# Kernel optimization log

Hardware: AMD Instinct MI355X
Metric: run time of the kernel (lower is better)

Reference implementation:

```python
import jax, jax.numpy as jnp
import numpy as np

B = 1048576          # batch size
N_IN = 10            # input features
NQ = 3               # n_qubits
NM = 2               # n_fuzzy_mem
NC = NM ** NQ        # 8 fuzzy combinations
EPS_GN = 1e-5
EPS_BN = 1e-5
CLAMP = 0.99999

# bit pattern per combination: loc[j] is the j-th digit (MSB first) of i in binary
SEL = jnp.array([[(i >> 2) & 1, (i >> 1) & 1, i & 1] for i in range(NC)], dtype=jnp.int32)  # [8,3]


def setup_inputs() -> dict:
    key = jax.random.key(0)
    ks = jax.random.split(key, 12)
    x = jax.random.normal(ks[0], (B, N_IN), dtype=jnp.float32)
    # linear 10->3 (xavier-ish scale), bias init 0.01 per weights_init
    W1 = jax.random.normal(ks[1], (NQ, N_IN), dtype=jnp.float32) * (1.0 / np.sqrt(N_IN))
    b1 = jnp.full((NQ,), 0.01, dtype=jnp.float32)
    # GroupNorm(1,3) affine
    gamma = jnp.ones((NQ,), dtype=jnp.float32)
    beta = jnp.zeros((NQ,), dtype=jnp.float32)
    # fuzzy membership params m, theta ~ N(0,1), shape [n_qubits, n_fuzzy_mem]
    m = jax.random.normal(ks[2], (NQ, NM), dtype=jnp.float32)
    theta = jax.random.normal(ks[3], (NQ, NM), dtype=jnp.float32)
    # BatchNorm1d(8) affine
    gamma2 = jnp.ones((NC,), dtype=jnp.float32)
    beta2 = jnp.zeros((NC,), dtype=jnp.float32)
    # softmax_linear 8->10
    W2 = jax.random.normal(ks[4], (N_IN, NC), dtype=jnp.float32) * (1.0 / np.sqrt(NC))
    b2 = jnp.full((N_IN,), 0.01, dtype=jnp.float32)
    return {"x": x, "W1": W1, "b1": b1, "gamma": gamma, "beta": beta,
            "m": m, "theta": theta, "gamma2": gamma2, "beta2": beta2,
            "W2": W2, "b2": b2}


def reference(x, W1, b1, gamma, beta, m, theta, gamma2, beta2, W2, b2):
    # linear 10 -> 3
    h = x @ W1.T + b1                                   # [B,3]
    # GroupNorm(1,3): per-sample normalization over channels (biased var)
    mu = h.mean(axis=1, keepdims=True)
    var = ((h - mu) ** 2).mean(axis=1, keepdims=True)
    h = (h - mu) * jax.lax.rsqrt(var + EPS_GN) * gamma + beta
    # gaussian fuzzy memberships: [B, n_mem=2, n_qubits=3]
    mT = m.T[None]                                      # [1,2,3]
    tT = theta.T[None]                                  # [1,2,3]
    fuzzy = jnp.exp(-((h[:, None, :] - mT) ** 2) / (2.0 * tT ** 2))  # [B,2,3]
    # select membership per combination: q_in[b,i,j] = fuzzy[b, SEL[i,j], j]
    q_in = fuzzy[:, SEL, jnp.arange(NQ)]                # [B,8,3]
    # RY angle = 2*arcsin(clamp(sqrt(q+1e-16))); per-qubit P(|1>) = sin^2(angle/2)
    sq = jnp.clip(jnp.sqrt(q_in + 1e-16), None, CLAMP)
    p = sq * sq                                         # [B,8,3]
    # 5-qubit circuit RY,RY,RY + CCX(0,1,3) + CCX(2,3,4); probs[1] = P(q0=1,q1=0,q2=0)
    out = p[..., 0] * (1.0 - p[..., 1]) * (1.0 - p[..., 2])  # [B,8]
    # BatchNorm1d(8), training mode (batch stats, biased var)
    mu2 = out.mean(axis=0)
    var2 = ((out - mu2) ** 2).mean(axis=0)
    out = (out - mu2) * jax.lax.rsqrt(var2 + EPS_BN) * gamma2 + beta2
    # softmax_linear 8 -> 10
    logits = out @ W2.T + b2                            # [B,10]
    # q_defuzz: 3-qubit RY circuit on first 3 logits; probs[0..2]
    s = jnp.sin(logits[:, :NQ] * 0.5)
    pq = s * s                                          # P(q_i=1), [B,3]
    cq = 1.0 - pq
    res = jnp.stack([cq[:, 0] * cq[:, 1] * cq[:, 2],
                     pq[:, 0] * cq[:, 1] * cq[:, 2],
                     cq[:, 0] * pq[:, 1] * cq[:, 2]], axis=1)  # [B,3]
    return res
```

## Files before the change

kernel.cpp:

```cpp
#include <hip/hip_runtime.h>

#define NROWS   1048576
#define NPAIRS  (NROWS / 2)
#define PMAX    0.9999800001f

#define P1_BLOCKS 1024
#define P1_THREADS 256
#define P2_BLOCKS (NPAIRS / 256)

__device__ __forceinline__ void fill_w(float* w, int t,
        const float* __restrict__ W1, const float* __restrict__ b1,
        const float* __restrict__ gamma, const float* __restrict__ beta,
        const float* __restrict__ mm, const float* __restrict__ theta) {
    if (t < 30) w[t] = W1[t];
    else if (t < 33) w[t] = b1[t - 30];
    else if (t < 39) { int k = t - 33; w[t] = (mm[k] - beta[k >> 1]) / gamma[k >> 1]; }
    else if (t < 45) { int k = t - 39; float g = gamma[k >> 1], th = theta[k];
                       w[t] = g * g / (2.0f * th * th); }
}

__device__ __forceinline__ void row_out(const float* xr, const float* w, float* o) {
    float h0 = w[30], h1 = w[31], h2 = w[32];
#pragma unroll
    for (int i = 0; i < 10; ++i) {
        h0 = fmaf(xr[i], w[i],      h0);
        h1 = fmaf(xr[i], w[10 + i], h1);
        h2 = fmaf(xr[i], w[20 + i], h2);
    }
    float mu = (h0 + h1 + h2) * (1.0f / 3.0f);
    float d0 = h0 - mu, d1 = h1 - mu, d2 = h2 - mu;
    float rs = rsqrtf((d0 * d0 + d1 * d1 + d2 * d2) * (1.0f / 3.0f) + 1e-5f);
    float u[3] = {d0 * rs, d1 * rs, d2 * rs};
    float P[3][2];
#pragma unroll
    for (int q = 0; q < 3; ++q)
#pragma unroll
        for (int s = 0; s < 2; ++s) {
            float d = u[q] - w[33 + q * 2 + s];
            float e = __expf(-(d * d) * w[39 + q * 2 + s]);
            P[q][s] = fminf(e + 1e-16f, PMAX);
        }
    float A0 = P[0][0], A1 = P[0][1];
    float B0 = 1.0f - P[1][0], B1 = 1.0f - P[1][1];
    float C0 = 1.0f - P[2][0], C1 = 1.0f - P[2][1];
    o[0] = A0 * B0 * C0; o[1] = A0 * B0 * C1; o[2] = A0 * B1 * C0; o[3] = A0 * B1 * C1;
    o[4] = A1 * B0 * C0; o[5] = A1 * B0 * C1; o[6] = A1 * B1 * C0; o[7] = A1 * B1 * C1;
}

__device__ __forceinline__ void load_pair(const float* __restrict__ x, int p, float* xr) {
    const float4* xv = reinterpret_cast<const float4*>(x) + (size_t)p * 5;
    float4 v0 = xv[0], v1 = xv[1], v2 = xv[2], v3 = xv[3], v4 = xv[4];
    xr[0] = v0.x; xr[1] = v0.y; xr[2] = v0.z; xr[3] = v0.w;
    xr[4] = v1.x; xr[5] = v1.y; xr[6] = v1.z; xr[7] = v1.w;
    xr[8] = v2.x; xr[9] = v2.y; xr[10] = v2.z; xr[11] = v2.w;
    xr[12] = v3.x; xr[13] = v3.y; xr[14] = v3.z; xr[15] = v3.w;
    xr[16] = v4.x; xr[17] = v4.y; xr[18] = v4.z; xr[19] = v4.w;
}

__global__ __launch_bounds__(256) void k_pass1(const float* __restrict__ x,
        const float* __restrict__ W1, const float* __restrict__ b1,
        const float* __restrict__ gamma, const float* __restrict__ beta,
        const float* __restrict__ mm, const float* __restrict__ theta,
        float* __restrict__ ws) {
    __shared__ float w[45];
    __shared__ float red[256][17];
    __shared__ float red2[16][17];
    int t = threadIdx.x;
    fill_w(w, t, W1, b1, gamma, beta, mm, theta);
    __syncthreads();

    float rw[45];
#pragma unroll
    for (int i = 0; i < 45; ++i) rw[i] = w[i];

    float s[8], ss[8];
#pragma unroll
    for (int c = 0; c < 8; ++c) { s[c] = 0.0f; ss[c] = 0.0f; }

    int tid = blockIdx.x * P1_THREADS + t;
    const int nthreads = P1_BLOCKS * P1_THREADS;
#pragma unroll
    for (int it = 0; it < 2; ++it) {
        int p = tid + it * nthreads;
        float xr[20];
        load_pair(x, p, xr);
        float o[8];
        row_out(xr, rw, o);
#pragma unroll
        for (int c = 0; c < 8; ++c) { s[c] += o[c]; ss[c] = fmaf(o[c], o[c], ss[c]); }
        row_out(xr + 10, rw, o);
#pragma unroll
        for (int c = 0; c < 8; ++c) { s[c] += o[c]; ss[c] = fmaf(o[c], o[c], ss[c]); }
    }

#pragma unroll
    for (int c = 0; c < 8; ++c) { red[t][c] = s[c]; red[t][8 + c] = ss[c]; }
    __syncthreads();
    {
        int c16 = t & 15, g = t >> 4;
        float partial = 0.0f;
#pragma unroll
        for (int j = 0; j < 16; ++j) partial += red[g * 16 + j][c16];
        red2[g][c16] = partial;
    }
    __syncthreads();
    if (t < 16) {
        float f = 0.0f;
#pragma unroll
        for (int g = 0; g < 16; ++g) f += red2[g][t];
        atomicAdd(&ws[(blockIdx.x & 15) * 16 + t], f);
    }
}

__global__ __launch_bounds__(256) void k_pass2(const float* __restrict__ x,
        const float* __restrict__ W1, const float* __restrict__ b1,
        const float* __restrict__ gamma, const float* __restrict__ beta,
        const float* __restrict__ mm, const float* __restrict__ theta,
        const float* __restrict__ g2, const float* __restrict__ be2,
        const float* __restrict__ W2, const float* __restrict__ b2,
        const float* __restrict__ ws, float* __restrict__ res) {
    __shared__ float w[45];
    __shared__ float weff[27];
    __shared__ float a8[8], sh8[8];
    int t = threadIdx.x;
    fill_w(w, t, W1, b1, gamma, beta, mm, theta);
    if (t >= 64 && t < 72) {
        int c = t - 64;
        float sv = 0.0f, qv = 0.0f;
#pragma unroll
        for (int r = 0; r < 16; ++r) { sv += ws[r * 16 + c]; qv += ws[r * 16 + 8 + c]; }
        const float invB = 1.0f / (float)NROWS;
        float mu = sv * invB;
        float var = qv * invB - mu * mu;
        float ac = g2[c] * rsqrtf(var + 1e-5f);
        a8[c] = ac;
        sh8[c] = be2[c] - mu * ac;
    }
    __syncthreads();
    if (t < 3) {
        float c0 = b2[t];
#pragma unroll
        for (int c = 0; c < 8; ++c) {
            float wv = W2[t * 8 + c];
            weff[t * 8 + c] = wv * a8[c];
            c0 += wv * sh8[c];
        }
        weff[24 + t] = c0;
    }
    __syncthreads();

    int p = blockIdx.x * 256 + t;
    float xr[20];
    load_pair(x, p, xr);
    float r[6];
#pragma unroll
    for (int rr = 0; rr < 2; ++rr) {
        float o[8];
        row_out(xr + rr * 10, w, o);
        float lg[3];
#pragma unroll
        for (int j = 0; j < 3; ++j) {
            float acc = weff[24 + j];
#pragma unroll
            for (int c = 0; c < 8; ++c) acc = fmaf(o[c], weff[j * 8 + c], acc);
            lg[j] = acc;
        }
        float s0 = __sinf(0.5f * lg[0]), s1 = __sinf(0.5f * lg[1]), s2 = __sinf(0.5f * lg[2]);
        float pq0 = s0 * s0, pq1 = s1 * s1, pq2 = s2 * s2;
        float cq0 = 1.0f - pq0, cq1 = 1.0f - pq1, cq2 = 1.0f - pq2;
        r[rr * 3 + 0] = cq0 * cq1 * cq2;
        r[rr * 3 + 1] = pq0 * cq1 * cq2;
        r[rr * 3 + 2] = cq0 * pq1 * cq2;
    }
    float2* ro = reinterpret_cast<float2*>(res + (size_t)p * 6);
    ro[0] = make_float2(r[0], r[1]);
    ro[1] = make_float2(r[2], r[3]);
    ro[2] = make_float2(r[4], r[5]);
}

extern "C" void kernel_launch(void* const* d_in, const int* in_sizes, int n_in,
                              void* d_out, int out_size, void* d_ws, size_t ws_size,
                              hipStream_t stream) {
    const float* x     = (const float*)d_in[0];
    const float* W1    = (const float*)d_in[1];
    const float* b1    = (const float*)d_in[2];
    const float* gamma = (const float*)d_in[3];
    const float* beta  = (const float*)d_in[4];
    const float* m     = (const float*)d_in[5];
    const float* theta = (const float*)d_in[6];
    const float* g2    = (const float*)d_in[7];
    const float* be2   = (const float*)d_in[8];
    const float* W2    = (const float*)d_in[9];
    const float* b2    = (const float*)d_in[10];
    float* ws  = (float*)d_ws;
    float* res = (float*)d_out;

    hipMemsetAsync(ws, 0, 16 * 16 * sizeof(float), stream);
    hipLaunchKernelGGL(k_pass1, dim3(P1_BLOCKS), dim3(P1_THREADS), 0, stream,
                       x, W1, b1, gamma, beta, m, theta, ws);
    hipLaunchKernelGGL(k_pass2, dim3(P2_BLOCKS), dim3(256), 0, stream,
                       x, W1, b1, gamma, beta, m, theta, g2, be2, W2, b2, ws, res);
}
```

Before: 116.2 us.

## Cache normalized per-row features from pass1 to avoid re-reading x in pass2

Pass 1 now stores the three GroupNorm-normalized features per row into the workspace, and pass 2 reads them instead of reloading the 10-feature input and recomputing the linear layer and normalization. This cuts pass 2 input traffic from 40 to 12 bytes per row and removes duplicated compute. The cost is an extra 12 bytes per row written in pass 1, and it relies on the workspace being large enough for the intermediate buffer.

```diff
diff --git a/kernel.cpp b/kernel.cpp
--- a/kernel.cpp
+++ b/kernel.cpp
@@ -6,7 +6,8 @@
 
 #define P1_BLOCKS 1024
 #define P1_THREADS 256
-#define P2_BLOCKS (NPAIRS / 256)
+#define P2_BLOCKS 2048
+#define UWS_OFF 256
 
 __device__ __forceinline__ void fill_w(float* w, int t,
         const float* __restrict__ W1, const float* __restrict__ b1,
@@ -19,7 +20,7 @@
                        w[t] = g * g / (2.0f * th * th); }
 }
 
-__device__ __forceinline__ void row_out(const float* xr, const float* w, float* o) {
+__device__ __forceinline__ void row_u(const float* xr, const float* w, float* u) {
     float h0 = w[30], h1 = w[31], h2 = w[32];
 #pragma unroll
     for (int i = 0; i < 10; ++i) {
@@ -30,7 +31,10 @@
     float mu = (h0 + h1 + h2) * (1.0f / 3.0f);
     float d0 = h0 - mu, d1 = h1 - mu, d2 = h2 - mu;
     float rs = rsqrtf((d0 * d0 + d1 * d1 + d2 * d2) * (1.0f / 3.0f) + 1e-5f);
-    float u[3] = {d0 * rs, d1 * rs, d2 * rs};
+    u[0] = d0 * rs; u[1] = d1 * rs; u[2] = d2 * rs;
+}
+
+__device__ __forceinline__ void o_from_u(const float* u, const float* w, float* o) {
     float P[3][2];
 #pragma unroll
     for (int q = 0; q < 3; ++q)
@@ -47,28 +51,17 @@
     o[4] = A1 * B0 * C0; o[5] = A1 * B0 * C1; o[6] = A1 * B1 * C0; o[7] = A1 * B1 * C1;
 }
 
-__device__ __forceinline__ void load_pair(const float* __restrict__ x, int p, float* xr) {
-    const float4* xv = reinterpret_cast<const float4*>(x) + (size_t)p * 5;
-    float4 v0 = xv[0], v1 = xv[1], v2 = xv[2], v3 = xv[3], v4 = xv[4];
-    xr[0] = v0.x; xr[1] = v0.y; xr[2] = v0.z; xr[3] = v0.w;
-    xr[4] = v1.x; xr[5] = v1.y; xr[6] = v1.z; xr[7] = v1.w;
-    xr[8] = v2.x; xr[9] = v2.y; xr[10] = v2.z; xr[11] = v2.w;
-    xr[12] = v3.x; xr[13] = v3.y; xr[14] = v3.z; xr[15] = v3.w;
-    xr[16] = v4.x; xr[17] = v4.y; xr[18] = v4.z; xr[19] = v4.w;
-}
-
 __global__ __launch_bounds__(256) void k_pass1(const float* __restrict__ x,
         const float* __restrict__ W1, const float* __restrict__ b1,
         const float* __restrict__ gamma, const float* __restrict__ beta,
         const float* __restrict__ mm, const float* __restrict__ theta,
         float* __restrict__ ws) {
     __shared__ float w[45];
-    __shared__ float red[256][17];
-    __shared__ float red2[16][17];
+    __shared__ float red[256 * 17];
+    __shared__ float red2[16 * 17];
     int t = threadIdx.x;
     fill_w(w, t, W1, b1, gamma, beta, mm, theta);
     __syncthreads();
-
     float rw[45];
 #pragma unroll
     for (int i = 0; i < 45; ++i) rw[i] = w[i];
@@ -77,42 +70,53 @@
 #pragma unroll
     for (int c = 0; c < 8; ++c) { s[c] = 0.0f; ss[c] = 0.0f; }
 
+    const float4* xv = reinterpret_cast<const float4*>(x);
+    float* uws = ws + UWS_OFF;
     int tid = blockIdx.x * P1_THREADS + t;
     const int nthreads = P1_BLOCKS * P1_THREADS;
 #pragma unroll
     for (int it = 0; it < 2; ++it) {
-        int p = tid + it * nthreads;
-        float xr[20];
-        load_pair(x, p, xr);
-        float o[8];
-        row_out(xr, rw, o);
+        size_t p = (size_t)tid + (size_t)it * nthreads;
+        const float4* xp = xv + p * 5;
+        float4 v0 = xp[0], v1 = xp[1], v2 = xp[2], v3 = xp[3], v4 = xp[4];
+        float xr[20] = {v0.x, v0.y, v0.z, v0.w, v1.x, v1.y, v1.z, v1.w,
+                        v2.x, v2.y, v2.z, v2.w, v3.x, v3.y, v3.z, v3.w,
+                        v4.x, v4.y, v4.z, v4.w};
+        float u0[3], u1[3], o[8];
+        row_u(xr, rw, u0);
+        o_from_u(u0, rw, o);
 #pragma unroll
         for (int c = 0; c < 8; ++c) { s[c] += o[c]; ss[c] = fmaf(o[c], o[c], ss[c]); }
-        row_out(xr + 10, rw, o);
+        row_u(xr + 10, rw, u1);
+        o_from_u(u1, rw, o);
 #pragma unroll
         for (int c = 0; c < 8; ++c) { s[c] += o[c]; ss[c] = fmaf(o[c], o[c], ss[c]); }
-    }
-
-#pragma unroll
-    for (int c = 0; c < 8; ++c) { red[t][c] = s[c]; red[t][8 + c] = ss[c]; }
+        float2* up = reinterpret_cast<float2*>(uws + p * 6);
+        up[0] = make_float2(u0[0], u0[1]);
+        up[1] = make_float2(u0[2], u1[0]);
+        up[2] = make_float2(u1[1], u1[2]);
+    }
+
+#pragma unroll
+    for (int c = 0; c < 8; ++c) { red[t * 17 + c] = s[c]; red[t * 17 + 8 + c] = ss[c]; }
     __syncthreads();
     {
         int c16 = t & 15, g = t >> 4;
         float partial = 0.0f;
 #pragma unroll
-        for (int j = 0; j < 16; ++j) partial += red[g * 16 + j][c16];
-        red2[g][c16] = partial;
+        for (int j = 0; j < 16; ++j) partial += red[(g * 16 + j) * 17 + c16];
+        red2[g * 17 + c16] = partial;
     }
     __syncthreads();
     if (t < 16) {
         float f = 0.0f;
 #pragma unroll
-        for (int g = 0; g < 16; ++g) f += red2[g][t];
+        for (int g = 0; g < 16; ++g) f += red2[g * 17 + t];
         atomicAdd(&ws[(blockIdx.x & 15) * 16 + t], f);
     }
 }
 
-__global__ __launch_bounds__(256) void k_pass2(const float* __restrict__ x,
+__global__ __launch_bounds__(256) void k_pass2(
         const float* __restrict__ W1, const float* __restrict__ b1,
         const float* __restrict__ gamma, const float* __restrict__ beta,
         const float* __restrict__ mm, const float* __restrict__ theta,
@@ -149,14 +153,18 @@
     }
     __syncthreads();
 
-    int p = blockIdx.x * 256 + t;
-    float xr[20];
-    load_pair(x, p, xr);
+    const float* uws = ws + UWS_OFF;
+    size_t p = (size_t)blockIdx.x * 256 + t;
+    const float2* up = reinterpret_cast<const float2*>(uws + p * 6);
+    float2 a = up[0], bb = up[1], cc = up[2];
+    float u0[3] = {a.x, a.y, bb.x};
+    float u1[3] = {bb.y, cc.x, cc.y};
+
     float r[6];
 #pragma unroll
     for (int rr = 0; rr < 2; ++rr) {
         float o[8];
-        row_out(xr + rr * 10, w, o);
+        o_from_u(rr ? u1 : u0, w, o);
         float lg[3];
 #pragma unroll
         for (int j = 0; j < 3; ++j) {
@@ -172,7 +180,7 @@
         r[rr * 3 + 1] = pq0 * cq1 * cq2;
         r[rr * 3 + 2] = cq0 * pq1 * cq2;
     }
-    float2* ro = reinterpret_cast<float2*>(res + (size_t)p * 6);
+    float2* ro = reinterpret_cast<float2*>(res + p * 6);
     ro[0] = make_float2(r[0], r[1]);
     ro[1] = make_float2(r[2], r[3]);
     ro[2] = make_float2(r[4], r[5]);
@@ -195,9 +203,9 @@
     float* ws  = (float*)d_ws;
     float* res = (float*)d_out;
 
-    hipMemsetAsync(ws, 0, 16 * 16 * sizeof(float), stream);
+    hipMemsetAsync(ws, 0, 256 * sizeof(float), stream);
     hipLaunchKernelGGL(k_pass1, dim3(P1_BLOCKS), dim3(P1_THREADS), 0, stream,
                        x, W1, b1, gamma, beta, m, theta, ws);
     hipLaunchKernelGGL(k_pass2, dim3(P2_BLOCKS), dim3(256), 0, stream,
-                       x, W1, b1, gamma, beta, m, theta, g2, be2, W2, b2, ws, res);
-}
+                       W1, b1, gamma, beta, m, theta, g2, be2, W2, b2, ws, res);
+}
```

After: 113.8 us. 1.02x faster.
